# Kernel optimization log

Hardware: AMD Instinct MI355X
Metric: run time of the kernel (lower is better)

Reference implementation:

```python
import jax, jax.numpy as jnp
import numpy as np

QUERY_DIM, FEAT_DIM, HID_DIM, OUT_DIM = 512, 2048, 512, 512
B, L, S, T = 8, 128, 100, 100


def setup_inputs() -> dict:
    key = jax.random.key(0)
    ks = jax.random.split(key, 9)
    d = {
        "query": jax.random.normal(ks[0], (B, L, QUERY_DIM), jnp.float32),
        "src": jax.random.normal(ks[1], (B, S, FEAT_DIM), jnp.float32),
        "trg": jax.random.normal(ks[2], (B, T, FEAT_DIM), jnp.float32),
        # params (LinearAct == Linear + identity act); src/trg projections share weights
        "Wq": jax.random.normal(ks[3], (QUERY_DIM, HID_DIM), jnp.float32) / np.sqrt(QUERY_DIM),
        "bq": jnp.zeros((HID_DIM,), jnp.float32),
        "Ws": jax.random.normal(ks[4], (FEAT_DIM, HID_DIM), jnp.float32) / np.sqrt(FEAT_DIM),
        "bs": jnp.zeros((HID_DIM,), jnp.float32),
        "Wo": jax.random.normal(ks[5], (HID_DIM + QUERY_DIM, OUT_DIM), jnp.float32) / np.sqrt(HID_DIM + QUERY_DIM),
        "bo": jnp.zeros((OUT_DIM,), jnp.float32),
    }
    return d


def reference(query, src, trg, Wq, bq, Ws, bs, Wo, bo):
    b, l, _ = query.shape
    s = src.shape[1]
    t = trg.shape[1]
    q = query @ Wq + bq          # b,l,k
    s_key = src @ Ws + bs        # b,s,k
    t_key = trg @ Ws + bs        # b,t,k
    hid = q.shape[-1]
    # score[b,l,s,t] = q . (s_key - t_key)/sqrt(2) / sqrt(hid) -- decomposed, no b,s,t,k tensor
    qs = jnp.einsum('blk,bsk->bls', q, s_key)
    qt = jnp.einsum('blk,btk->blt', q, t_key)
    score = (qs[:, :, :, None] - qt[:, :, None, :]) / jnp.sqrt(jnp.asarray(2.0 * hid, q.dtype))
    w = jax.nn.softmax(score.reshape(b, l, s * t), axis=-1).reshape(b, l, s, t)
    # ctx = sum_{s,t} w * (s_key - t_key)/sqrt(2), decomposed via marginals
    ws = w.sum(axis=3)           # b,l,s
    wt = w.sum(axis=2)           # b,l,t
    ctx = (jnp.einsum('bls,bsk->blk', ws, s_key) - jnp.einsum('blt,btk->blk', wt, t_key)) / jnp.sqrt(jnp.asarray(2.0, q.dtype))
    x = jnp.concatenate([query, ctx], axis=-1) @ Wo + bo
    return x
```

## Files before the change

### kernel.cpp

```cpp
#include <hip/hip_runtime.h>
#include <math.h>


typedef __attribute__((ext_vector_type(8))) short s16x8;
typedef __attribute__((ext_vector_type(4))) float f32x4;

__device__ __forceinline__ unsigned short f2bf(float f) {
    unsigned int u = __float_as_uint(f);
    return (unsigned short)((u + 0x7fffu + ((u >> 16) & 1u)) >> 16);
}

__device__ __forceinline__ s16x8 cvt8(const float* p) {
    float4 u = *(const float4*)p, w = *(const float4*)(p + 4);
    s16x8 o;
    o[0] = (short)f2bf(u.x); o[1] = (short)f2bf(u.y);
    o[2] = (short)f2bf(u.z); o[3] = (short)f2bf(u.w);
    o[4] = (short)f2bf(w.x); o[5] = (short)f2bf(w.y);
    o[6] = (short)f2bf(w.z); o[7] = (short)f2bf(w.w);
    return o;
}

__global__ __launch_bounds__(256) void k_prep(
    const float* __restrict__ Wq, const float* __restrict__ Ws,
    const float* __restrict__ Wo,
    unsigned short* __restrict__ WqT, unsigned short* __restrict__ WsT,
    unsigned short* __restrict__ WoT, float* __restrict__ keys) {
    __shared__ float tile[32][33];
    const int bid = blockIdx.x, t = threadIdx.x;

    if (bid < 1792) {
        const int id = bid;
        const float* W; unsigned short* O; int K, tk, tn;
        if (id < 256)       { W = Wq; O = WqT; K = 512;  tk = id >> 4;          tn = id & 15; }
        else if (id < 1280) { W = Ws; O = WsT; K = 2048; tk = (id - 256) >> 4;  tn = (id - 256) & 15; }
        else                { W = Wo; O = WoT; K = 1024; tk = (id - 1280) >> 4; tn = (id - 1280) & 15; }
        const int row = t >> 3, c4 = (t & 7) * 4;
        float4 v = *(const float4*)(W + (size_t)(tk * 32 + row) * 512 + tn * 32 + c4);
        tile[row][c4 + 0] = v.x; tile[row][c4 + 1] = v.y;
        tile[row][c4 + 2] = v.z; tile[row][c4 + 3] = v.w;
        __syncthreads();
        ushort4 o = make_ushort4(f2bf(tile[c4 + 0][row]), f2bf(tile[c4 + 1][row]),
                                 f2bf(tile[c4 + 2][row]), f2bf(tile[c4 + 3][row]));
        *(ushort4*)(O + (size_t)(tn * 32 + row) * K + tk * 32 + c4) = o;
    } else {
        const int f = ((bid - 1792) * 256 + t) * 4;
        *(float4*)(keys + f) = make_float4(0.f, 0.f, 0.f, 0.f);
    }
}

__device__ __forceinline__ void gemm64_keys(
    const float* __restrict__ src, const float* __restrict__ trg,
    const unsigned short* __restrict__ BT, float* __restrict__ C,
    int m0, int n0, int kbase, unsigned short* As, unsigned short* Bs) {
    const int t = threadIdx.x;
    const int lane = t & 63, wid = t >> 6;
    const int wm = (wid & 1) * 32, wn = (wid >> 1) * 32;
    const int lr = lane & 15, lq = lane >> 4;
    const int r = t >> 3, c8 = (t & 7) * 8;

    const int ra_row = m0 + r, rb_row = m0 + r + 32;
    const float* arp = (ra_row < 800) ? (src + (size_t)ra_row * 2048)
                                      : (trg + (size_t)(ra_row - 800) * 2048);
    const float* brp = (rb_row < 800) ? (src + (size_t)rb_row * 2048)
                                      : (trg + (size_t)(rb_row - 800) * 2048);

    s16x8 ra0, ra1, rb0, rb1;
#define LDK(kt)                                                            \
    ra0 = cvt8(arp + (kt) + c8);                                           \
    ra1 = cvt8(brp + (kt) + c8);                                           \
    rb0 = *(const s16x8*)(BT + (size_t)(n0 + r)      * 2048 + (kt) + c8);  \
    rb1 = *(const s16x8*)(BT + (size_t)(n0 + r + 32) * 2048 + (kt) + c8);

    f32x4 acc[2][2] = {};
    LDK(kbase);
    for (int it = 0; it < 16; it++) {
        __syncthreads();
        *(s16x8*)&As[r * 72 + c8]        = ra0;
        *(s16x8*)&As[(r + 32) * 72 + c8] = ra1;
        *(s16x8*)&Bs[r * 72 + c8]        = rb0;
        *(s16x8*)&Bs[(r + 32) * 72 + c8] = rb1;
        __syncthreads();
        if (it < 15) { LDK(kbase + (it + 1) * 64); }
#pragma unroll
        for (int s = 0; s < 2; s++) {
            s16x8 a0 = *(const s16x8*)&As[(wm + lr) * 72      + s * 32 + lq * 8];
            s16x8 a1 = *(const s16x8*)&As[(wm + 16 + lr) * 72 + s * 32 + lq * 8];
            s16x8 b0 = *(const s16x8*)&Bs[(wn + lr) * 72      + s * 32 + lq * 8];
            s16x8 b1 = *(const s16x8*)&Bs[(wn + 16 + lr) * 72 + s * 32 + lq * 8];
            acc[0][0] = __builtin_amdgcn_mfma_f32_16x16x32_bf16(a0, b0, acc[0][0], 0, 0, 0);
            acc[0][1] = __builtin_amdgcn_mfma_f32_16x16x32_bf16(a0, b1, acc[0][1], 0, 0, 0);
            acc[1][0] = __builtin_amdgcn_mfma_f32_16x16x32_bf16(a1, b0, acc[1][0], 0, 0, 0);
            acc[1][1] = __builtin_amdgcn_mfma_f32_16x16x32_bf16(a1, b1, acc[1][1], 0, 0, 0);
        }
    }
#undef LDK
#pragma unroll
    for (int i = 0; i < 2; i++)
#pragma unroll
        for (int j = 0; j < 2; j++) {
            const int col = n0 + wn + j * 16 + lr;
            const int row = m0 + wm + i * 16 + lq * 4;
#pragma unroll
            for (int rr = 0; rr < 4; rr++)
                unsafeAtomicAdd(&C[(size_t)(row + rr) * 512 + col], acc[i][j][rr]);
        }
}

__device__ __forceinline__ void gemm64_P(
    const float* __restrict__ keys, const unsigned short* __restrict__ wotBot,
    float* __restrict__ P, int m0, int n0, unsigned short* As,
    unsigned short* Bs) {
    const int t = threadIdx.x;
    const int lane = t & 63, wid = t >> 6;
    const int wm = (wid & 1) * 32, wn = (wid >> 1) * 32;
    const int lr = lane & 15, lq = lane >> 4;
    const int r = t >> 3, c8 = (t & 7) * 8;

    s16x8 ra0, ra1, rb0, rb1;
#define LDP(kt)                                                               \
    ra0 = cvt8(keys + (size_t)(m0 + r)      * 512 + (kt) + c8);               \
    ra1 = cvt8(keys + (size_t)(m0 + r + 32) * 512 + (kt) + c8);               \
    rb0 = *(const s16x8*)(wotBot + (size_t)(n0 + r)      * 1024 + (kt) + c8); \
    rb1 = *(const s16x8*)(wotBot + (size_t)(n0 + r + 32) * 1024 + (kt) + c8);

    f32x4 acc[2][2] = {};
    LDP(0);
    for (int it = 0; it < 8; it++) {
        __syncthreads();
        *(s16x8*)&As[r * 72 + c8]        = ra0;
        *(s16x8*)&As[(r + 32) * 72 + c8] = ra1;
        *(s16x8*)&Bs[r * 72 + c8]        = rb0;
        *(s16x8*)&Bs[(r + 32) * 72 + c8] = rb1;
        __syncthreads();
        if (it < 7) { LDP((it + 1) * 64); }
#pragma unroll
        for (int s = 0; s < 2; s++) {
            s16x8 a0 = *(const s16x8*)&As[(wm + lr) * 72      + s * 32 + lq * 8];
            s16x8 a1 = *(const s16x8*)&As[(wm + 16 + lr) * 72 + s * 32 + lq * 8];
            s16x8 b0 = *(const s16x8*)&Bs[(wn + lr) * 72      + s * 32 + lq * 8];
            s16x8 b1 = *(const s16x8*)&Bs[(wn + 16 + lr) * 72 + s * 32 + lq * 8];
            acc[0][0] = __builtin_amdgcn_mfma_f32_16x16x32_bf16(a0, b0, acc[0][0], 0, 0, 0);
            acc[0][1] = __builtin_amdgcn_mfma_f32_16x16x32_bf16(a0, b1, acc[0][1], 0, 0, 0);
            acc[1][0] = __builtin_amdgcn_mfma_f32_16x16x32_bf16(a1, b0, acc[1][0], 0, 0, 0);
            acc[1][1] = __builtin_amdgcn_mfma_f32_16x16x32_bf16(a1, b1, acc[1][1], 0, 0, 0);
        }
    }
#undef LDP
#pragma unroll
    for (int i = 0; i < 2; i++)
#pragma unroll
        for (int j = 0; j < 2; j++) {
            const int col = n0 + wn + j * 16 + lr;
            const int row = m0 + wm + i * 16 + lq * 4;
#pragma unroll
            for (int rr = 0; rr < 4; rr++)
                P[(size_t)(row + rr) * 512 + col] = acc[i][j][rr];
        }
}

template <int MODE>
__device__ __forceinline__ void gemm32(
    const float* __restrict__ A, const unsigned short* __restrict__ BT,
    const float* __restrict__ bias, void* __restrict__ Cv,
    int m0, int n0, int KA, int KB, int N, int kiters,
    unsigned short* As, unsigned short* Bs) {
    const int t = threadIdx.x;
    const int lane = t & 63, wid = t >> 6;
    const int wm = (wid & 1) * 16, wn = (wid >> 1) * 32;
    const int lr = lane & 15, lq = lane >> 4;
    const int r = t >> 3, c8 = (t & 7) * 8;

    s16x8 ra, rb0, rb1;
#define LD32(kt)                                                            \
    ra  = cvt8(A + (size_t)(m0 + r) * KA + (kt) + c8);                      \
    rb0 = *(const s16x8*)(BT + (size_t)(n0 + r)      * KB + (kt) + c8);     \
    rb1 = *(const s16x8*)(BT + (size_t)(n0 + r + 32) * KB + (kt) + c8);

    f32x4 acc[2] = {};
    LD32(0);
    for (int it = 0; it < kiters; it++) {
        __syncthreads();
        *(s16x8*)&As[r * 72 + c8]        = ra;
        *(s16x8*)&Bs[r * 72 + c8]        = rb0;
        *(s16x8*)&Bs[(r + 32) * 72 + c8] = rb1;
        __syncthreads();
        if (it + 1 < kiters) { LD32((it + 1) * 64); }
#pragma unroll
        for (int s = 0; s < 2; s++) {
            s16x8 a0 = *(const s16x8*)&As[(wm + lr) * 72      + s * 32 + lq * 8];
            s16x8 b0 = *(const s16x8*)&Bs[(wn + lr) * 72      + s * 32 + lq * 8];
            s16x8 b1 = *(const s16x8*)&Bs[(wn + 16 + lr) * 72 + s * 32 + lq * 8];
            acc[0] = __builtin_amdgcn_mfma_f32_16x16x32_bf16(a0, b0, acc[0], 0, 0, 0);
            acc[1] = __builtin_amdgcn_mfma_f32_16x16x32_bf16(a0, b1, acc[1], 0, 0, 0);
        }
    }
#undef LD32
#pragma unroll
    for (int j = 0; j < 2; j++) {
        const int col = n0 + wn + j * 16 + lr;
        const int row = m0 + wm + lq * 4;
        const float bv = bias[col];
        if (MODE == 0) {
            float* C = (float*)Cv;
#pragma unroll
            for (int rr = 0; rr < 4; rr++)
                C[(size_t)(row + rr) * N + col] = acc[j][rr] + bv;
        } else {
            unsigned short* C = (unsigned short*)Cv;
#pragma unroll
            for (int rr = 0; rr < 4; rr++)
                C[(size_t)(row + rr) * N + col] = f2bf(acc[j][rr] + bv);
        }
    }
}

__global__ __launch_bounds__(256) void k_stageB(
    const float* __restrict__ query, const float* __restrict__ src,
    const float* __restrict__ trg, const unsigned short* __restrict__ WqT,
    const unsigned short* __restrict__ WsT, const unsigned short* __restrict__ WoT,
    const float* __restrict__ bq, const float* __restrict__ bo,
    unsigned short* __restrict__ qh, float* __restrict__ keys,
    float* __restrict__ out) {
    __shared__ __align__(16) unsigned short As[64 * 72];
    __shared__ __align__(16) unsigned short Bs[64 * 72];
    const int bid = blockIdx.x;
    if (bid < 400) {
        const int c = bid / 200, rem = bid % 200;
        const int mt = rem >> 3, nt = rem & 7;
        gemm64_keys(src, trg, WsT, keys, mt * 64, nt * 64, c * 1024, As, Bs);
    } else if (bid < 656) {
        const int r = bid - 400;
        const int mt = r >> 3, nt = r & 7;
        gemm32<2>(query, WqT, bq, qh, mt * 32, nt * 64, 512, 512, 512,
                  8, As, Bs);
    } else {
        const int r = bid - 656;
        const int mt = r >> 3, nt = r & 7;
        gemm32<0>(query, WoT, bo, out, mt * 32, nt * 64, 512, 1024, 512,
                  8, As, Bs);
    }
}

__global__ __launch_bounds__(256) void k_stageC(
    const unsigned short* __restrict__ qh, const float* __restrict__ keys,
    const unsigned short* __restrict__ wotBot, float* __restrict__ sc,
    float* __restrict__ P) {
    __shared__ __align__(16) unsigned short As[64 * 72];
    __shared__ __align__(16) unsigned short Bs[64 * 72];
    const int bid = blockIdx.x;
    const int t = threadIdx.x;

    if (bid >= 128) {
        const int rem = bid - 128;
        gemm64_P(keys, wotBot, P, (rem >> 3) * 64, (rem & 7) * 64, As, Bs);
        return;
    }

    const int mt = bid >> 2, nt = bid & 3;
    const int m0 = mt * 32, b = mt >> 2, n0 = nt * 64;
    const int lane = t & 63, wid = t >> 6;
    const int wm = (wid & 1) * 16, wn = (wid >> 1) * 32;
    const int lr = lane & 15, lq = lane >> 4;
    const int r = t >> 3, c8 = (t & 7) * 8;

    const int nA = n0 + r, nB = n0 + r + 32;
    int kr0 = (nA < 128) ? (b * 100 + nA) : (800 + b * 100 + (nA - 128));
    int kr1 = (nB < 128) ? (b * 100 + nB) : (800 + b * 100 + (nB - 128));
    kr0 = kr0 > 1599 ? 1599 : kr0;
    kr1 = kr1 > 1599 ? 1599 : kr1;

    s16x8 ra, rb0, rb1;
#define LDSC(kt)                                                    \
    ra  = *(const s16x8*)(qh + (size_t)(m0 + r) * 512 + (kt) + c8); \
    rb0 = cvt8(keys + (size_t)kr0 * 512 + (kt) + c8);               \
    rb1 = cvt8(keys + (size_t)kr1 * 512 + (kt) + c8);

    f32x4 acc[2] = {};
    LDSC(0);
    for (int it = 0; it < 8; it++) {
        __syncthreads();
        *(s16x8*)&As[r * 72 + c8]        = ra;
        *(s16x8*)&Bs[r * 72 + c8]        = rb0;
        *(s16x8*)&Bs[(r + 32) * 72 + c8] = rb1;
        __syncthreads();
        if (it < 7) { LDSC((it + 1) * 64); }
#pragma unroll
        for (int s = 0; s < 2; s++) {
            s16x8 a0 = *(const s16x8*)&As[(wm + lr) * 72      + s * 32 + lq * 8];
            s16x8 b0 = *(const s16x8*)&Bs[(wn + lr) * 72      + s * 32 + lq * 8];
            s16x8 b1 = *(const s16x8*)&Bs[(wn + 16 + lr) * 72 + s * 32 + lq * 8];
            acc[0] = __builtin_amdgcn_mfma_f32_16x16x32_bf16(a0, b0, acc[0], 0, 0, 0);
            acc[1] = __builtin_amdgcn_mfma_f32_16x16x32_bf16(a0, b1, acc[1], 0, 0, 0);
        }
    }
#undef LDSC
#pragma unroll
    for (int j = 0; j < 2; j++) {
        const int col = n0 + wn + j * 16 + lr;
        const int row = m0 + wm + lq * 4;
        const float scale = (col >= 128) ? -(1.0f / 32.0f) : (1.0f / 32.0f);
#pragma unroll
        for (int rr = 0; rr < 4; rr++)
            sc[(size_t)(row + rr) * 256 + col] = acc[j][rr] * scale;
    }
}

__global__ __launch_bounds__(256) void k_stageD(
    const float* __restrict__ sc, const float* __restrict__ P,
    float* __restrict__ out) {
    __shared__ float wbuf[200 * 33];
    __shared__ float Bs[40 * 32];

    const int t = threadIdx.x;
    const int b = blockIdx.y;
    const int n0 = blockIdx.x * 32;
    const int l0 = blockIdx.z * 32;
    const int wave = t >> 6, lane = t & 63;

    for (int i = 0; i < 8; i++) {
        const int li = wave * 8 + i;
        const float4 v = *(const float4*)(
            sc + (size_t)(b * 128 + l0 + li) * 256 + lane * 4);
        const float vv[4] = {v.x, v.y, v.z, v.w};
        const int c0 = lane * 4;
        float mS = -1e30f, mT = -1e30f;
#pragma unroll
        for (int j = 0; j < 4; j++) {
            const int col = c0 + j;
            if (col < 100) mS = fmaxf(mS, vv[j]);
            if (col >= 128 && col < 228) mT = fmaxf(mT, vv[j]);
        }
#pragma unroll
        for (int off = 32; off > 0; off >>= 1) {
            mS = fmaxf(mS, __shfl_xor(mS, off));
            mT = fmaxf(mT, __shfl_xor(mT, off));
        }
        float eS[4], eT[4], sS = 0.f, sT = 0.f;
#pragma unroll
        for (int j = 0; j < 4; j++) {
            const int col = c0 + j;
            eS[j] = (col < 100) ? __expf(vv[j] - mS) : 0.f;
            eT[j] = (col >= 128 && col < 228) ? __expf(vv[j] - mT) : 0.f;
            sS += eS[j]; sT += eT[j];
        }
#pragma unroll
        for (int off = 32; off > 0; off >>= 1) {
            sS += __shfl_xor(sS, off);
            sT += __shfl_xor(sT, off);
        }
        const float iS = 1.f / sS, iT = 1.f / sT;
#pragma unroll
        for (int j = 0; j < 4; j++) {
            const int col = c0 + j;
            if (col < 100) wbuf[col * 33 + li] = eS[j] * iS;
            if (col >= 128 && col < 228)
                wbuf[(100 + col - 128) * 33 + li] = eT[j] * iT;
        }
    }
    __syncthreads();

    const int tx = t & 7, ty = t >> 3;
    float rB[5];
    auto loadB = [&](int kbase) {
#pragma unroll
        for (int e = 0; e < 5; e++) {
            const int idx = t + e * 256;
            const int k = idx >> 5, j = idx & 31;
            const int kk = kbase + k;
            rB[e] = (kk < 100)
                ?  P[(size_t)(b * 100 + kk) * 512 + n0 + j]
                : -P[(size_t)(800 + b * 100 + (kk - 100)) * 512 + n0 + j];
        }
    };

    float acc[4] = {};
    loadB(0);
    for (int c5 = 0; c5 < 5; c5++) {
        __syncthreads();
#pragma unroll
        for (int e = 0; e < 5; e++) {
            const int idx = t + e * 256;
            Bs[idx] = rB[e];
        }
        __syncthreads();
        if (c5 < 4) loadB((c5 + 1) * 40);
#pragma unroll 8
        for (int k = 0; k < 40; k++) {
            const float ar = wbuf[(c5 * 40 + k) * 33 + ty];
            float br[4];
            *(float4*)br = *(const float4*)&Bs[k * 32 + tx * 4];
#pragma unroll
            for (int j = 0; j < 4; j++) acc[j] = fmaf(ar, br[j], acc[j]);
        }
    }

    const float s2 = 0.70710678118654752f;
    const int m = b * 128 + l0 + ty;
#pragma unroll
    for (int j = 0; j < 4; j++)
        unsafeAtomicAdd(&out[(size_t)m * 512 + n0 + tx * 4 + j], acc[j] * s2);
}


extern "C" void kernel_launch(void* const* d_in, const int* in_sizes, int n_in,
                              void* d_out, int out_size, void* d_ws, size_t ws_size,
                              hipStream_t stream) {
    const float* query = (const float*)d_in[0];
    const float* src   = (const float*)d_in[1];
    const float* trg   = (const float*)d_in[2];
    const float* Wq    = (const float*)d_in[3];
    const float* bq    = (const float*)d_in[4];
    const float* Ws    = (const float*)d_in[5];
    const float* Wo    = (const float*)d_in[7];
    const float* bo    = (const float*)d_in[8];
    float* out = (float*)d_out;

    float* keys = (float*)d_ws;
    float* sc   = keys + 819200;
    float* P    = sc   + 262144;
    unsigned short* qh  = (unsigned short*)(P + 819200);
    unsigned short* wqt = qh  + 524288;
    unsigned short* wst = wqt + 262144;
    unsigned short* wot = wst + 1048576;

    k_prep<<<2592, 256, 0, stream>>>(Wq, Ws, Wo, wqt, wst, wot, keys);
    k_stageB<<<912, 256, 0, stream>>>(query, src, trg, wqt, wst, wot, bq, bo,
                                      qh, keys, out);
    k_stageC<<<328, 256, 0, stream>>>(qh, keys, wot + 512, sc, P);
    k_stageD<<<dim3(16, 8, 4), 256, 0, stream>>>(sc, P, out);
}
```

Measured before the change: 130.7 us.

## Fuse weight transpose and bf16 conversion into GEMM tile loads, drop prep kernel

Removes the separate prep kernel that transposed and converted Wq, Ws and Wo to bf16. Each GEMM now reads the fp32 row-major weights directly with float4 loads and transposes them into shared memory while converting. The keys buffer is zeroed with hipMemsetAsync instead. This saves a launch and a round-trip write and read of the weight copies, but it reads fp32 weights (twice the bytes) in every tile, adds conversion work per block, and the transposed shared-memory writes may hit bank conflicts.

```diff
diff --git a/kernel.cpp b/kernel.cpp
--- a/kernel.cpp
+++ b/kernel.cpp
@@ -20,56 +20,45 @@
     return o;
 }
 
-__global__ __launch_bounds__(256) void k_prep(
-    const float* __restrict__ Wq, const float* __restrict__ Ws,
-    const float* __restrict__ Wo,
-    unsigned short* __restrict__ WqT, unsigned short* __restrict__ WsT,
-    unsigned short* __restrict__ WoT, float* __restrict__ keys) {
-    __shared__ float tile[32][33];
-    const int bid = blockIdx.x, t = threadIdx.x;
-
-    if (bid < 1792) {
-        const int id = bid;
-        const float* W; unsigned short* O; int K, tk, tn;
-        if (id < 256)       { W = Wq; O = WqT; K = 512;  tk = id >> 4;          tn = id & 15; }
-        else if (id < 1280) { W = Ws; O = WsT; K = 2048; tk = (id - 256) >> 4;  tn = (id - 256) & 15; }
-        else                { W = Wo; O = WoT; K = 1024; tk = (id - 1280) >> 4; tn = (id - 1280) & 15; }
-        const int row = t >> 3, c4 = (t & 7) * 4;
-        float4 v = *(const float4*)(W + (size_t)(tk * 32 + row) * 512 + tn * 32 + c4);
-        tile[row][c4 + 0] = v.x; tile[row][c4 + 1] = v.y;
-        tile[row][c4 + 2] = v.z; tile[row][c4 + 3] = v.w;
-        __syncthreads();
-        ushort4 o = make_ushort4(f2bf(tile[c4 + 0][row]), f2bf(tile[c4 + 1][row]),
-                                 f2bf(tile[c4 + 2][row]), f2bf(tile[c4 + 3][row]));
-        *(ushort4*)(O + (size_t)(tn * 32 + row) * K + tk * 32 + c4) = o;
-    } else {
-        const int f = ((bid - 1792) * 256 + t) * 4;
-        *(float4*)(keys + f) = make_float4(0.f, 0.f, 0.f, 0.f);
-    }
+__device__ __forceinline__ void wr4x4(unsigned short* Bs, int c4, int kr0,
+                                      float4 w0, float4 w1, float4 w2, float4 w3) {
+    *(ushort4*)&Bs[(c4 + 0) * 72 + kr0] =
+        make_ushort4(f2bf(w0.x), f2bf(w1.x), f2bf(w2.x), f2bf(w3.x));
+    *(ushort4*)&Bs[(c4 + 1) * 72 + kr0] =
+        make_ushort4(f2bf(w0.y), f2bf(w1.y), f2bf(w2.y), f2bf(w3.y));
+    *(ushort4*)&Bs[(c4 + 2) * 72 + kr0] =
+        make_ushort4(f2bf(w0.z), f2bf(w1.z), f2bf(w2.z), f2bf(w3.z));
+    *(ushort4*)&Bs[(c4 + 3) * 72 + kr0] =
+        make_ushort4(f2bf(w0.w), f2bf(w1.w), f2bf(w2.w), f2bf(w3.w));
 }
 
 __device__ __forceinline__ void gemm64_keys(
     const float* __restrict__ src, const float* __restrict__ trg,
-    const unsigned short* __restrict__ BT, float* __restrict__ C,
+    const float* __restrict__ Ws, float* __restrict__ C,
     int m0, int n0, int kbase, unsigned short* As, unsigned short* Bs) {
     const int t = threadIdx.x;
     const int lane = t & 63, wid = t >> 6;
     const int wm = (wid & 1) * 32, wn = (wid >> 1) * 32;
     const int lr = lane & 15, lq = lane >> 4;
     const int r = t >> 3, c8 = (t & 7) * 8;
+    const int kr0 = (t >> 4) * 4, c4 = (t & 15) * 4;
 
     const int ra_row = m0 + r, rb_row = m0 + r + 32;
     const float* arp = (ra_row < 800) ? (src + (size_t)ra_row * 2048)
                                       : (trg + (size_t)(ra_row - 800) * 2048);
     const float* brp = (rb_row < 800) ? (src + (size_t)rb_row * 2048)
                                       : (trg + (size_t)(rb_row - 800) * 2048);
-
-    s16x8 ra0, ra1, rb0, rb1;
-#define LDK(kt)                                                            \
-    ra0 = cvt8(arp + (kt) + c8);                                           \
-    ra1 = cvt8(brp + (kt) + c8);                                           \
-    rb0 = *(const s16x8*)(BT + (size_t)(n0 + r)      * 2048 + (kt) + c8);  \
-    rb1 = *(const s16x8*)(BT + (size_t)(n0 + r + 32) * 2048 + (kt) + c8);
+    const float* wp = Ws + n0 + c4;
+
+    s16x8 ra0, ra1;
+    float4 w0, w1, w2, w3;
+#define LDK(kt)                                                  \
+    ra0 = cvt8(arp + (kt) + c8);                                 \
+    ra1 = cvt8(brp + (kt) + c8);                                 \
+    w0 = *(const float4*)(wp + (size_t)((kt) + kr0 + 0) * 512);  \
+    w1 = *(const float4*)(wp + (size_t)((kt) + kr0 + 1) * 512);  \
+    w2 = *(const float4*)(wp + (size_t)((kt) + kr0 + 2) * 512);  \
+    w3 = *(const float4*)(wp + (size_t)((kt) + kr0 + 3) * 512);
 
     f32x4 acc[2][2] = {};
     LDK(kbase);
@@ -77,8 +66,7 @@
         __syncthreads();
         *(s16x8*)&As[r * 72 + c8]        = ra0;
         *(s16x8*)&As[(r + 32) * 72 + c8] = ra1;
-        *(s16x8*)&Bs[r * 72 + c8]        = rb0;
-        *(s16x8*)&Bs[(r + 32) * 72 + c8] = rb1;
+        wr4x4(Bs, c4, kr0, w0, w1, w2, w3);
         __syncthreads();
         if (it < 15) { LDK(kbase + (it + 1) * 64); }
 #pragma unroll
@@ -107,7 +95,7 @@
 }
 
 __device__ __forceinline__ void gemm64_P(
-    const float* __restrict__ keys, const unsigned short* __restrict__ wotBot,
+    const float* __restrict__ keys, const float* __restrict__ WoBot,
     float* __restrict__ P, int m0, int n0, unsigned short* As,
     unsigned short* Bs) {
     const int t = threadIdx.x;
@@ -115,13 +103,18 @@
     const int wm = (wid & 1) * 32, wn = (wid >> 1) * 32;
     const int lr = lane & 15, lq = lane >> 4;
     const int r = t >> 3, c8 = (t & 7) * 8;
-
-    s16x8 ra0, ra1, rb0, rb1;
-#define LDP(kt)                                                               \
-    ra0 = cvt8(keys + (size_t)(m0 + r)      * 512 + (kt) + c8);               \
-    ra1 = cvt8(keys + (size_t)(m0 + r + 32) * 512 + (kt) + c8);               \
-    rb0 = *(const s16x8*)(wotBot + (size_t)(n0 + r)      * 1024 + (kt) + c8); \
-    rb1 = *(const s16x8*)(wotBot + (size_t)(n0 + r + 32) * 1024 + (kt) + c8);
+    const int kr0 = (t >> 4) * 4, c4 = (t & 15) * 4;
+    const float* wp = WoBot + n0 + c4;
+
+    s16x8 ra0, ra1;
+    float4 w0, w1, w2, w3;
+#define LDP(kt)                                                  \
+    ra0 = cvt8(keys + (size_t)(m0 + r)      * 512 + (kt) + c8);  \
+    ra1 = cvt8(keys + (size_t)(m0 + r + 32) * 512 + (kt) + c8);  \
+    w0 = *(const float4*)(wp + (size_t)((kt) + kr0 + 0) * 512);  \
+    w1 = *(const float4*)(wp + (size_t)((kt) + kr0 + 1) * 512);  \
+    w2 = *(const float4*)(wp + (size_t)((kt) + kr0 + 2) * 512);  \
+    w3 = *(const float4*)(wp + (size_t)((kt) + kr0 + 3) * 512);
 
     f32x4 acc[2][2] = {};
     LDP(0);
@@ -129,8 +122,7 @@
         __syncthreads();
         *(s16x8*)&As[r * 72 + c8]        = ra0;
         *(s16x8*)&As[(r + 32) * 72 + c8] = ra1;
-        *(s16x8*)&Bs[r * 72 + c8]        = rb0;
-        *(s16x8*)&Bs[(r + 32) * 72 + c8] = rb1;
+        wr4x4(Bs, c4, kr0, w0, w1, w2, w3);
         __syncthreads();
         if (it < 7) { LDP((it + 1) * 64); }
 #pragma unroll
@@ -159,32 +151,35 @@
 }
 
 template <int MODE>
-__device__ __forceinline__ void gemm32(
-    const float* __restrict__ A, const unsigned short* __restrict__ BT,
+__device__ __forceinline__ void gemm32w(
+    const float* __restrict__ A, const float* __restrict__ W,
     const float* __restrict__ bias, void* __restrict__ Cv,
-    int m0, int n0, int KA, int KB, int N, int kiters,
-    unsigned short* As, unsigned short* Bs) {
+    int m0, int n0, unsigned short* As, unsigned short* Bs) {
     const int t = threadIdx.x;
     const int lane = t & 63, wid = t >> 6;
     const int wm = (wid & 1) * 16, wn = (wid >> 1) * 32;
     const int lr = lane & 15, lq = lane >> 4;
     const int r = t >> 3, c8 = (t & 7) * 8;
-
-    s16x8 ra, rb0, rb1;
-#define LD32(kt)                                                            \
-    ra  = cvt8(A + (size_t)(m0 + r) * KA + (kt) + c8);                      \
-    rb0 = *(const s16x8*)(BT + (size_t)(n0 + r)      * KB + (kt) + c8);     \
-    rb1 = *(const s16x8*)(BT + (size_t)(n0 + r + 32) * KB + (kt) + c8);
+    const int kr0 = (t >> 4) * 4, c4 = (t & 15) * 4;
+    const float* wp = W + n0 + c4;
+
+    s16x8 ra;
+    float4 w0, w1, w2, w3;
+#define LD32(kt)                                                 \
+    ra = cvt8(A + (size_t)(m0 + r) * 512 + (kt) + c8);           \
+    w0 = *(const float4*)(wp + (size_t)((kt) + kr0 + 0) * 512);  \
+    w1 = *(const float4*)(wp + (size_t)((kt) + kr0 + 1) * 512);  \
+    w2 = *(const float4*)(wp + (size_t)((kt) + kr0 + 2) * 512);  \
+    w3 = *(const float4*)(wp + (size_t)((kt) + kr0 + 3) * 512);
 
     f32x4 acc[2] = {};
     LD32(0);
-    for (int it = 0; it < kiters; it++) {
-        __syncthreads();
-        *(s16x8*)&As[r * 72 + c8]        = ra;
-        *(s16x8*)&Bs[r * 72 + c8]        = rb0;
-        *(s16x8*)&Bs[(r + 32) * 72 + c8] = rb1;
-        __syncthreads();
-        if (it + 1 < kiters) { LD32((it + 1) * 64); }
+    for (int it = 0; it < 8; it++) {
+        __syncthreads();
+        *(s16x8*)&As[r * 72 + c8] = ra;
+        wr4x4(Bs, c4, kr0, w0, w1, w2, w3);
+        __syncthreads();
+        if (it < 7) { LD32((it + 1) * 64); }
 #pragma unroll
         for (int s = 0; s < 2; s++) {
             s16x8 a0 = *(const s16x8*)&As[(wm + lr) * 72      + s * 32 + lq * 8];
@@ -204,20 +199,20 @@
             float* C = (float*)Cv;
 #pragma unroll
             for (int rr = 0; rr < 4; rr++)
-                C[(size_t)(row + rr) * N + col] = acc[j][rr] + bv;
+                C[(size_t)(row + rr) * 512 + col] = acc[j][rr] + bv;
         } else {
             unsigned short* C = (unsigned short*)Cv;
 #pragma unroll
             for (int rr = 0; rr < 4; rr++)
-                C[(size_t)(row + rr) * N + col] = f2bf(acc[j][rr] + bv);
+                C[(size_t)(row + rr) * 512 + col] = f2bf(acc[j][rr] + bv);
         }
     }
 }
 
 __global__ __launch_bounds__(256) void k_stageB(
     const float* __restrict__ query, const float* __restrict__ src,
-    const float* __restrict__ trg, const unsigned short* __restrict__ WqT,
-    const unsigned short* __restrict__ WsT, const unsigned short* __restrict__ WoT,
+    const float* __restrict__ trg, const float* __restrict__ Wq,
+    const float* __restrict__ Ws, const float* __restrict__ Wo,
     const float* __restrict__ bq, const float* __restrict__ bo,
     unsigned short* __restrict__ qh, float* __restrict__ keys,
     float* __restrict__ out) {
@@ -227,23 +222,21 @@
     if (bid < 400) {
         const int c = bid / 200, rem = bid % 200;
         const int mt = rem >> 3, nt = rem & 7;
-        gemm64_keys(src, trg, WsT, keys, mt * 64, nt * 64, c * 1024, As, Bs);
+        gemm64_keys(src, trg, Ws, keys, mt * 64, nt * 64, c * 1024, As, Bs);
     } else if (bid < 656) {
         const int r = bid - 400;
         const int mt = r >> 3, nt = r & 7;
-        gemm32<2>(query, WqT, bq, qh, mt * 32, nt * 64, 512, 512, 512,
-                  8, As, Bs);
+        gemm32w<2>(query, Wq, bq, qh, mt * 32, nt * 64, As, Bs);
     } else {
         const int r = bid - 656;
         const int mt = r >> 3, nt = r & 7;
-        gemm32<0>(query, WoT, bo, out, mt * 32, nt * 64, 512, 1024, 512,
-                  8, As, Bs);
+        gemm32w<0>(query, Wo, bo, out, mt * 32, nt * 64, As, Bs);
     }
 }
 
 __global__ __launch_bounds__(256) void k_stageC(
     const unsigned short* __restrict__ qh, const float* __restrict__ keys,
-    const unsigned short* __restrict__ wotBot, float* __restrict__ sc,
+    const float* __restrict__ WoBot, float* __restrict__ sc,
     float* __restrict__ P) {
     __shared__ __align__(16) unsigned short As[64 * 72];
     __shared__ __align__(16) unsigned short Bs[64 * 72];
@@ -252,7 +245,7 @@
 
     if (bid >= 128) {
         const int rem = bid - 128;
-        gemm64_P(keys, wotBot, P, (rem >> 3) * 64, (rem & 7) * 64, As, Bs);
+        gemm64_P(keys, WoBot, P, (rem >> 3) * 64, (rem & 7) * 64, As, Bs);
         return;
     }
 
@@ -418,14 +411,11 @@
     float* keys = (float*)d_ws;
     float* sc   = keys + 819200;
     float* P    = sc   + 262144;
-    unsigned short* qh  = (unsigned short*)(P + 819200);
-    unsigned short* wqt = qh  + 524288;
-    unsigned short* wst = wqt + 262144;
-    unsigned short* wot = wst + 1048576;
-
-    k_prep<<<2592, 256, 0, stream>>>(Wq, Ws, Wo, wqt, wst, wot, keys);
-    k_stageB<<<912, 256, 0, stream>>>(query, src, trg, wqt, wst, wot, bq, bo,
+    unsigned short* qh = (unsigned short*)(P + 819200);
+
+    hipMemsetAsync(keys, 0, 819200 * sizeof(float), stream);
+    k_stageB<<<912, 256, 0, stream>>>(query, src, trg, Wq, Ws, Wo, bq, bo,
                                       qh, keys, out);
-    k_stageC<<<328, 256, 0, stream>>>(qh, keys, wot + 512, sc, P);
+    k_stageC<<<328, 256, 0, stream>>>(qh, keys, Wo + 512 * 512, sc, P);
     k_stageD<<<dim3(16, 8, 4), 256, 0, stream>>>(sc, P, out);
 }
```

Result: slower. 139.0 us (+6.4%).
